# Kernel optimization log

Measured on AMD Instinct MI355X. Metric: run time of the kernel, lower is better.

The kernel has to match this reference:

```python
import jax, jax.numpy as jnp
import numpy as np

N_NODES = 10000
N_EDGES = 160000
HID = 256
NBOND = 6
NATOM = 62
NLAYERS = 6


def _lin_init(key, fan_in, fan_out):
    # torch nn.Linear default: U(-1/sqrt(fan_in), 1/sqrt(fan_in))
    kw, kb = jax.random.split(key)
    bound = 1.0 / np.sqrt(fan_in)
    w = jax.random.uniform(kw, (fan_in, fan_out), jnp.float32, -bound, bound)
    b = jax.random.uniform(kb, (fan_out,), jnp.float32, -bound, bound)
    return w, b


def setup_inputs() -> dict:
    key = jax.random.key(0)
    ks = jax.random.split(key, 32)
    atom_features = jax.random.normal(ks[0], (N_NODES, NATOM), jnp.float32)
    edge_index = jax.random.randint(ks[1], (2, N_EDGES), 0, N_NODES, jnp.int64 if jax.config.jax_enable_x64 else jnp.int32)
    edge_features = jax.random.normal(ks[2], (N_EDGES, NBOND), jnp.float32)

    embed_w, embed_b = _lin_init(ks[3], NATOM, HID)

    msg_in = 2 * HID + NBOND  # 518
    mw1, mb1, mw2, mb2 = [], [], [], []
    uw1, ub1, uw2, ub2 = [], [], [], []
    for i in range(NLAYERS):
        k = jax.random.split(ks[4 + i], 4)
        w, b = _lin_init(k[0], msg_in, HID); mw1.append(w); mb1.append(b)
        w, b = _lin_init(k[1], HID, HID); mw2.append(w); mb2.append(b)
        w, b = _lin_init(k[2], 2 * HID, HID); uw1.append(w); ub1.append(b)
        w, b = _lin_init(k[3], HID, HID); uw2.append(w); ub2.append(b)

    r_w1, r_b1 = _lin_init(ks[20], HID, HID)
    r_w2, r_b2 = _lin_init(ks[21], HID, HID // 2)
    r_w3, r_b3 = _lin_init(ks[22], HID // 2, 1)

    return {
        "atom_features": atom_features,
        "edge_index": edge_index,
        "edge_features": edge_features,
        "embed_w": embed_w, "embed_b": embed_b,
        "msg_w1": jnp.stack(mw1), "msg_b1": jnp.stack(mb1),
        "msg_w2": jnp.stack(mw2), "msg_b2": jnp.stack(mb2),
        "upd_w1": jnp.stack(uw1), "upd_b1": jnp.stack(ub1),
        "upd_w2": jnp.stack(uw2), "upd_b2": jnp.stack(ub2),
        "r_w1": r_w1, "r_b1": r_b1,
        "r_w2": r_w2, "r_b2": r_b2,
        "r_w3": r_w3, "r_b3": r_b3,
    }


def _mlp2(x, w1, b1, w2, b2):
    return jnp.maximum(x @ w1 + b1, 0.0) @ w2 + b2


def reference(atom_features, edge_index, edge_features,
              embed_w, embed_b,
              msg_w1, msg_b1, msg_w2, msg_b2,
              upd_w1, upd_b1, upd_w2, upd_b2,
              r_w1, r_b1, r_w2, r_b2, r_w3, r_b3):
    src, dst = edge_index[0], edge_index[1]
    n = atom_features.shape[0]
    x = atom_features @ embed_w + embed_b  # [N, H]
    for l in range(msg_w1.shape[0]):
        # per-edge gather + concat -> message MLP
        msg_in = jnp.concatenate([x[src], x[dst], edge_features], axis=-1)  # [E, 2H+B]
        msgs = _mlp2(msg_in, msg_w1[l], msg_b1[l], msg_w2[l], msg_b2[l])  # [E, H]
        # scatter-add into dst nodes
        agg = jax.ops.segment_sum(msgs, dst, num_segments=n)  # [N, H]
        x = _mlp2(jnp.concatenate([x, agg], axis=-1), upd_w1[l], upd_b1[l], upd_w2[l], upd_b2[l])
    # readout (dropout is identity in eval mode)
    h = jnp.maximum(x @ r_w1 + r_b1, 0.0)
    h = jnp.maximum(h @ r_w2 + r_b2, 0.0)
    out = h @ r_w3 + r_b3  # [N, 1]
    return out.mean(axis=0)  # [1]
```

## Files before the change

### kernel.cpp

```cpp
#include <hip/hip_runtime.h>
#include <hip/hip_bf16.h>
#include <hip/hip_fp16.h>


#define HID 256

typedef _Float16 h8 __attribute__((ext_vector_type(8)));
typedef float f32x4 __attribute__((ext_vector_type(4)));

__device__ __forceinline__ void unpack_h8(const int4& r, float* f) {
    const __half2* h = reinterpret_cast<const __half2*>(&r);
#pragma unroll
    for (int k = 0; k < 4; ++k) {
        float2 t = __half22float2(h[k]);
        f[2 * k] = t.x;
        f[2 * k + 1] = t.y;
    }
}

__device__ __forceinline__ void gld16(const void* g, void* l) {
    __builtin_amdgcn_global_load_lds(
        (const __attribute__((address_space(1))) void*)g,
        (__attribute__((address_space(3))) void*)l, 16, 0, 0);
}

__device__ __forceinline__ int swz(int row) { return (row + (row >> 2)) & 3; }


__global__ void hist_act_kernel(const int* __restrict__ dst, int* __restrict__ deg,
                                int E, const float* __restrict__ atom,
                                __half* __restrict__ atomH, int NA) {
    int i = blockIdx.x * blockDim.x + threadIdx.x;
    if (i < E) atomicAdd(&deg[dst[i]], 1);
    if (i < NA) {
        int r = i >> 3, seg = i & 7;
        h8 v;
#pragma unroll
        for (int j = 0; j < 8; ++j) {
            int c = seg * 8 + j;
            v[j] = (_Float16)((c < 62) ? atom[(size_t)r * 62 + c] : 0.f);
        }
        *reinterpret_cast<h8*>(&atomH[(size_t)r * 64 + seg * 8]) = v;
    }
}

__global__ __launch_bounds__(256) void scan_kernel(
    const int* __restrict__ deg, int* __restrict__ offs, float* __restrict__ degf, int n) {
    __shared__ int ws[4];
    const int t = threadIdx.x;
    const int lane = t & 63;
    const int w = t >> 6;
    const int per = (n + 255) / 256;
    const int s = t * per;
    const int e = min(s + per, n);
    int sum = 0;
    for (int i = s; i < e; ++i) sum += deg[i];
    int v = sum;
#pragma unroll
    for (int off = 1; off < 64; off <<= 1) {
        int u = __shfl_up(v, off, 64);
        if (lane >= off) v += u;
    }
    if (lane == 63) ws[w] = v;
    __syncthreads();
    if (t == 0) {
        int c = 0;
#pragma unroll
        for (int i = 0; i < 4; ++i) { int x = ws[i]; ws[i] = c; c += x; }
    }
    __syncthreads();
    int run = ws[w] + v - sum;
    for (int i = s; i < e; ++i) {
        int d = deg[i];
        offs[i] = run;
        degf[i] = (float)d;
        run += d;
    }
    if (e == n) offs[n] = run;
}


struct CDesc {
    const float* src;
    __half* dst;
    int Kreal, Kpad, srcN, tile0;
};
struct CTab {
    CDesc d[32];
    int nd;
};

__device__ void convert_body(const CTab& tab, int bid) {
    int idx = 0;
    for (int i = 1; i < tab.nd; ++i)
        if (tab.d[i].tile0 <= bid) idx = i;
    const CDesc d = tab.d[idx];
    const int q = bid - d.tile0;
    const int ntN = d.srcN >> 6;
    const int kb = (q / ntN) * 32;
    const int nb = (q % ntN) * 64;
    const int n = nb + (threadIdx.x & 63);
    const int k0 = kb + (threadIdx.x >> 6) * 8;
    h8 v;
#pragma unroll
    for (int j = 0; j < 8; ++j) {
        int k = k0 + j;
        v[j] = (_Float16)((k < d.Kreal) ? d.src[(size_t)k * d.srcN + n] : 0.f);
    }
    *reinterpret_cast<h8*>(&d.dst[(size_t)n * d.Kpad + k0]) = v;
}

__global__ __launch_bounds__(256) void scatter_conv_kernel(
    const int* __restrict__ src, const int* __restrict__ dst,
    const int* __restrict__ offs, int* __restrict__ cursor,
    int* __restrict__ csr_src, const float* __restrict__ ef,
    __half* __restrict__ ef8, int E, int sblocks, CTab tab) {
    if ((int)blockIdx.x < sblocks) {
        int i = blockIdx.x * blockDim.x + threadIdx.x;
        if (i < E) {
            int d = dst[i];
            int pos = atomicAdd(&cursor[d], 1);
            int idx = offs[d] + pos;
            csr_src[idx] = src[i];
            const float* s6 = ef + (size_t)i * 6;
            unsigned short h[8];
#pragma unroll
            for (int j = 0; j < 6; ++j) h[j] = __half_as_ushort(__float2half_rn(s6[j]));
            h[6] = 0; h[7] = 0;
            int4 pk;
            pk.x = (int)(h[0] | ((unsigned)h[1] << 16));
            pk.y = (int)(h[2] | ((unsigned)h[3] << 16));
            pk.z = (int)(h[4] | ((unsigned)h[5] << 16));
            pk.w = (int)(h[6] | ((unsigned)h[7] << 16));
            *reinterpret_cast<int4*>(ef8 + (size_t)idx * 8) = pk;
        }
    } else {
        convert_body(tab, blockIdx.x - sblocks);
    }
}


struct BDesc { float* out; const float* base; const float* v1; const float* B1;
               const float* v2; const float* B2; };
struct BTab { BDesc d[31]; };


#define ASTR 40

struct FDesc { const float* U2; const __half* Wfb; __half* dst; };
struct FTab { FDesc d[22]; };

__global__ __launch_bounds__(256) void fold_bias_kernel(FTab tab, BTab bt, int fblocks) {
    if ((int)blockIdx.x >= fblocks) {
        const BDesc d = bt.d[blockIdx.x - fblocks];
        const int j = threadIdx.x;
        float acc = d.base ? d.base[j] : 0.f;
        if (d.v1)
            for (int k = 0; k < 256; ++k) acc = fmaf(d.v1[k], d.B1[(size_t)k * 256 + j], acc);
        if (d.v2)
            for (int k = 0; k < 256; ++k) acc = fmaf(d.v2[k], d.B2[(size_t)k * 256 + j], acc);
        d.out[j] = acc;
        return;
    }
    const FDesc dd = tab.d[blockIdx.x >> 4];
    const int t4 = blockIdx.x & 15;
    const int rowBase = (t4 >> 2) * 64;
    const int colBase = (t4 & 3) * 64;

    __shared__ __align__(16) _Float16 Ah[64 * ASTR];
    __shared__ __align__(16) _Float16 Bh[64 * ASTR];

    const int tid = threadIdx.x;
    const int lane = tid & 63;
    const int wave = tid >> 6;
    const int waveM = (wave >> 1) * 32;
    const int waveN = (wave & 1) * 32;
    const int m0 = lane & 15;
    const int quad = lane >> 4;
    const int sr = tid >> 2;
    const int sseg = tid & 3;

    const f32x4 z = {0.f, 0.f, 0.f, 0.f};
    f32x4 acc[2][2] = {{z, z}, {z, z}};

    for (int kb = 0; kb < 256; kb += 32) {
        {
            size_t off = (size_t)(rowBase + sr) * 256 + kb + sseg * 8;
            *reinterpret_cast<int4*>(&Ah[sr * ASTR + sseg * 8]) =
                *reinterpret_cast<const int4*>(&dd.Wfb[off]);
        }
        {
            const float* Bp = dd.U2 + (size_t)(colBase + sr) * 256 + kb + sseg * 8;
            float4 u0 = *reinterpret_cast<const float4*>(Bp);
            float4 u1 = *reinterpret_cast<const float4*>(Bp + 4);
            h8 v;
            v[0] = (_Float16)u0.x; v[1] = (_Float16)u0.y;
            v[2] = (_Float16)u0.z; v[3] = (_Float16)u0.w;
            v[4] = (_Float16)u1.x; v[5] = (_Float16)u1.y;
            v[6] = (_Float16)u1.z; v[7] = (_Float16)u1.w;
            *reinterpret_cast<h8*>(&Bh[sr * ASTR + sseg * 8]) = v;
        }
        __syncthreads();

        const h8 a0 = *reinterpret_cast<const h8*>(&Ah[(waveM + m0) * ASTR + quad * 8]);
        const h8 a1 = *reinterpret_cast<const h8*>(&Ah[(waveM + 16 + m0) * ASTR + quad * 8]);
        const h8 b0 = *reinterpret_cast<const h8*>(&Bh[(waveN + m0) * ASTR + quad * 8]);
        const h8 b1 = *reinterpret_cast<const h8*>(&Bh[(waveN + 16 + m0) * ASTR + quad * 8]);

        acc[0][0] = __builtin_amdgcn_mfma_f32_16x16x32_f16(a0, b0, acc[0][0], 0, 0, 0);
        acc[0][1] = __builtin_amdgcn_mfma_f32_16x16x32_f16(a0, b1, acc[0][1], 0, 0, 0);
        acc[1][0] = __builtin_amdgcn_mfma_f32_16x16x32_f16(a1, b0, acc[1][0], 0, 0, 0);
        acc[1][1] = __builtin_amdgcn_mfma_f32_16x16x32_f16(a1, b1, acc[1][1], 0, 0, 0);

        __syncthreads();
    }

#pragma unroll
    for (int tm = 0; tm < 2; ++tm)
#pragma unroll
        for (int reg = 0; reg < 4; ++reg) {
            int n = rowBase + waveM + tm * 16 + quad * 4 + reg;
#pragma unroll
            for (int tn = 0; tn < 2; ++tn) {
                int k = colBase + waveN + tn * 16 + m0;
                dd.dst[(size_t)n * 256 + k] = __float2half_rn(acc[tm][tn][reg]);
            }
        }
}


template <int TN>
__global__ __launch_bounds__(256) void mfma_gemm(
    const __half* __restrict__ A, int lda,
    const __half* __restrict__ W, int K,
    const float* __restrict__ bias, const float* __restrict__ bias2,
    const float* __restrict__ rowscale,
    const __half* __restrict__ addend, int astride,
    __half* __restrict__ C, int M, int Nc, int do_relu) {
    constexpr int BUF = 4096 + TN * 2048;
    __shared__ __align__(16) unsigned char lds[2 * BUF];

    const int tid = threadIdx.x;
    const int lane = tid & 63;
    const int wave = tid >> 6;
    const int m0 = lane & 15;
    const int quad = lane >> 4;
    const int waveM = (wave >> 1) * 32;
    const int waveN = (wave & 1) * (TN * 16);
    const int rowBase = blockIdx.x * 64;
    const int colBase = blockIdx.y * (TN * 32);

    const int sa_r = tid >> 2;
    const int sa_ks = (tid & 3) ^ swz(sa_r);
    const int sa_row = min(rowBase + sa_r, M - 1);
    const int sb_r1 = sa_r + 64;
    const int sb_ks1 = (tid & 3) ^ swz(sb_r1);

    int aoff[2], boff[TN];
#pragma unroll
    for (int tm = 0; tm < 2; ++tm) {
        int r = waveM + tm * 16 + m0;
        aoff[tm] = ((r << 2) + (quad ^ swz(r))) << 4;
    }
#pragma unroll
    for (int tn = 0; tn < TN; ++tn) {
        int r = waveN + tn * 16 + m0;
        boff[tn] = 4096 + (((r << 2) + (quad ^ swz(r))) << 4);
    }

    const f32x4 z = {0.f, 0.f, 0.f, 0.f};
    f32x4 acc[2][TN];
#pragma unroll
    for (int tm = 0; tm < 2; ++tm)
#pragma unroll
        for (int tn = 0; tn < TN; ++tn) acc[tm][tn] = z;

    const __half* ga = A + (size_t)sa_row * lda + sa_ks * 8;
    const __half* gb0 = W + (size_t)(colBase + sa_r) * K + sa_ks * 8;
    const __half* gb1 = W + (size_t)(colBase + sb_r1) * K + sb_ks1 * 8;

    auto issue = [&](int p, int kb) {
        unsigned char* base = lds + p * BUF;
        gld16(ga + kb, base + wave * 1024);
        gld16(gb0 + kb, base + 4096 + wave * 1024);
        if constexpr (TN == 4) gld16(gb1 + kb, base + 8192 + wave * 1024);
    };

    issue(0, 0);
    int p = 0;
    for (int kb = 0; kb < K; kb += 32) {
        const bool has_next = (kb + 32 < K);
        if (has_next) issue(p ^ 1, kb + 32);
        if (has_next) {
            if constexpr (TN == 4)
                asm volatile("s_waitcnt vmcnt(3)" ::: "memory");
            else
                asm volatile("s_waitcnt vmcnt(2)" ::: "memory");
        } else {
            asm volatile("s_waitcnt vmcnt(0)" ::: "memory");
        }
        asm volatile("s_barrier" ::: "memory");

        const unsigned char* base = lds + p * BUF;
        h8 ah[2], bh[TN];
#pragma unroll
        for (int tm = 0; tm < 2; ++tm)
            ah[tm] = *reinterpret_cast<const h8*>(base + aoff[tm]);
#pragma unroll
        for (int tn = 0; tn < TN; ++tn)
            bh[tn] = *reinterpret_cast<const h8*>(base + boff[tn]);
#pragma unroll
        for (int tm = 0; tm < 2; ++tm)
#pragma unroll
            for (int tn = 0; tn < TN; ++tn)
                acc[tm][tn] = __builtin_amdgcn_mfma_f32_16x16x32_f16(
                    ah[tm], bh[tn], acc[tm][tn], 0, 0, 0);
        asm volatile("s_waitcnt lgkmcnt(0)" ::: "memory");
        asm volatile("s_barrier" ::: "memory");
        p ^= 1;
    }

    float cb[TN], db[TN];
    int col[TN];
#pragma unroll
    for (int tn = 0; tn < TN; ++tn) {
        col[tn] = colBase + waveN + tn * 16 + m0;
        cb[tn] = bias ? bias[col[tn]] : 0.f;
        db[tn] = bias2 ? bias2[col[tn]] : 0.f;
    }
#pragma unroll
    for (int tm = 0; tm < 2; ++tm) {
#pragma unroll
        for (int reg = 0; reg < 4; ++reg) {
            int row = rowBase + waveM + tm * 16 + quad * 4 + reg;
            if (row >= M) continue;
            float rs = rowscale ? rowscale[row] : 0.0f;
#pragma unroll
            for (int tn = 0; tn < TN; ++tn) {
                float v = acc[tm][tn][reg] + cb[tn] + rs * db[tn];
                if (addend)
                    v += __half2float(addend[(size_t)row * astride + col[tn]]);
                if (do_relu) v = fmaxf(v, 0.f);
                C[(size_t)row * Nc + col[tn]] = __float2half_rn(v);
            }
        }
    }
}


__global__ __launch_bounds__(256) void aggregate_kernel(
    const __half* __restrict__ PQ, const __half* __restrict__ ef8,
    const int* __restrict__ offs, const int* __restrict__ csr_src,
    const float* __restrict__ W1c, __half* __restrict__ Hagg, int n) {
    const int wave = threadIdx.x >> 6;
    const int lane = threadIdx.x & 63;
    const int node = blockIdx.x * 4 + wave;
    if (node >= n) return;
    const int hw = lane >> 5;
    const int sl = lane & 31;
    const int ch = sl * 8;

    float wc[6][8];
#pragma unroll
    for (int k = 0; k < 6; ++k) {
        float4 w0 = *reinterpret_cast<const float4*>(W1c + k * HID + ch);
        float4 w1 = *reinterpret_cast<const float4*>(W1c + k * HID + ch + 4);
        wc[k][0] = w0.x; wc[k][1] = w0.y; wc[k][2] = w0.z; wc[k][3] = w0.w;
        wc[k][4] = w1.x; wc[k][5] = w1.y; wc[k][6] = w1.z; wc[k][7] = w1.w;
    }
    float qb[8];
    {
        int4 r = *reinterpret_cast<const int4*>(PQ + (size_t)node * 768 + 256 + ch);
        unpack_h8(r, qb);
    }
    float acc[8] = {0.f, 0.f, 0.f, 0.f, 0.f, 0.f, 0.f, 0.f};

    auto fma_edge = [&](const int4& praw, const int4& eraw) {
        float p[8], e[8];
        unpack_h8(praw, p);
        unpack_h8(eraw, e);
#pragma unroll
        for (int i = 0; i < 8; ++i) {
            float h = p[i] + qb[i];
            h = fmaf(e[0], wc[0][i], h);
            h = fmaf(e[1], wc[1][i], h);
            h = fmaf(e[2], wc[2][i], h);
            h = fmaf(e[3], wc[3][i], h);
            h = fmaf(e[4], wc[4][i], h);
            h = fmaf(e[5], wc[5][i], h);
            acc[i] += fmaxf(h, 0.f);
        }
    };

    const int beg = offs[node];
    const int end = offs[node + 1];
    int j = beg + hw;

    while (j + 10 < end) {
        int s0 = csr_src[j];
        int s1 = csr_src[j + 2];
        int s2 = csr_src[j + 4];
        int s3 = csr_src[j + 6];
        int s4 = csr_src[j + 8];
        int s5 = csr_src[j + 10];
        int4 e0 = *reinterpret_cast<const int4*>(ef8 + (size_t)j * 8);
        int4 e1 = *reinterpret_cast<const int4*>(ef8 + (size_t)(j + 2) * 8);
        int4 e2 = *reinterpret_cast<const int4*>(ef8 + (size_t)(j + 4) * 8);
        int4 e3 = *reinterpret_cast<const int4*>(ef8 + (size_t)(j + 6) * 8);
        int4 e4 = *reinterpret_cast<const int4*>(ef8 + (size_t)(j + 8) * 8);
        int4 e5 = *reinterpret_cast<const int4*>(ef8 + (size_t)(j + 10) * 8);
        int4 p0 = *reinterpret_cast<const int4*>(PQ + (size_t)s0 * 768 + ch);
        int4 p1 = *reinterpret_cast<const int4*>(PQ + (size_t)s1 * 768 + ch);
        int4 p2 = *reinterpret_cast<const int4*>(PQ + (size_t)s2 * 768 + ch);
        int4 p3 = *reinterpret_cast<const int4*>(PQ + (size_t)s3 * 768 + ch);
        int4 p4 = *reinterpret_cast<const int4*>(PQ + (size_t)s4 * 768 + ch);
        int4 p5 = *reinterpret_cast<const int4*>(PQ + (size_t)s5 * 768 + ch);
        fma_edge(p0, e0);
        fma_edge(p1, e1);
        fma_edge(p2, e2);
        fma_edge(p3, e3);
        fma_edge(p4, e4);
        fma_edge(p5, e5);
        j += 12;
    }
    for (; j + 2 < end; j += 4) {
        int s0 = csr_src[j];
        int s1 = csr_src[j + 2];
        int4 e0 = *reinterpret_cast<const int4*>(ef8 + (size_t)j * 8);
        int4 e1 = *reinterpret_cast<const int4*>(ef8 + (size_t)(j + 2) * 8);
        int4 p0 = *reinterpret_cast<const int4*>(PQ + (size_t)s0 * 768 + ch);
        int4 p1 = *reinterpret_cast<const int4*>(PQ + (size_t)s1 * 768 + ch);
        fma_edge(p0, e0);
        fma_edge(p1, e1);
    }
    if (j < end) {
        int s = csr_src[j];
        int4 e = *reinterpret_cast<const int4*>(ef8 + (size_t)j * 8);
        int4 pw = *reinterpret_cast<const int4*>(PQ + (size_t)s * 768 + ch);
        fma_edge(pw, e);
    }

    unsigned short hs[8];
#pragma unroll
    for (int i = 0; i < 8; ++i) {
        float tot = acc[i] + __shfl_down(acc[i], 32, 64);
        hs[i] = __half_as_ushort(__float2half_rn(tot));
    }
    if (hw == 0) {
        int4 pk;
        pk.x = (int)(hs[0] | ((unsigned)hs[1] << 16));
        pk.y = (int)(hs[2] | ((unsigned)hs[3] << 16));
        pk.z = (int)(hs[4] | ((unsigned)hs[5] << 16));
        pk.w = (int)(hs[6] | ((unsigned)hs[7] << 16));
        *reinterpret_cast<int4*>(Hagg + (size_t)node * HID + ch) = pk;
    }
}


__global__ __launch_bounds__(256) void readout_kernel(
    const __half* __restrict__ U5, const __half* __restrict__ wF,
    const float* __restrict__ cbF, const __half* __restrict__ wR2,
    const float* __restrict__ bR2, const float* __restrict__ w3,
    const float* __restrict__ b3, float* __restrict__ accum,
    int* __restrict__ done, float* __restrict__ outp, int M, int nblocks) {
    __shared__ __align__(16) unsigned char lds[24576 + 64 * 272 * 2];
    _Float16* h1 = (_Float16*)(lds + 24576);

    const int tid = threadIdx.x;
    const int lane = tid & 63;
    const int wave = tid >> 6;
    const int m0 = lane & 15;
    const int quad = lane >> 4;
    const int waveM = (wave >> 1) * 32;
    const int waveN = (wave & 1) * 64;
    const int rowBase = blockIdx.x * 64;

    const int sa_r = tid >> 2;
    const int sa_ks = (tid & 3) ^ swz(sa_r);
    const int sa_row = min(rowBase + sa_r, M - 1);
    const int sb_r1 = sa_r + 64;
    const int sb_ks1 = (tid & 3) ^ swz(sb_r1);

    int aoff[2], boff[4];
#pragma unroll
    for (int tm = 0; tm < 2; ++tm) {
        int r = waveM + tm * 16 + m0;
        aoff[tm] = ((r << 2) + (quad ^ swz(r))) << 4;
    }
#pragma unroll
    for (int tn = 0; tn < 4; ++tn) {
        int r = waveN + tn * 16 + m0;
        boff[tn] = (((r << 2) + (quad ^ swz(r))) << 4);
    }

    constexpr int BUF = 4096 + 4 * 2048;
    const f32x4 z = {0.f, 0.f, 0.f, 0.f};

    for (int half = 0; half < 2; ++half) {
        const __half* W = wF + (size_t)(half * 128) * 256;
        f32x4 acc[2][4] = {{z, z, z, z}, {z, z, z, z}};
        const __half* ga = U5 + (size_t)sa_row * 256 + sa_ks * 8;
        const __half* gb0 = W + (size_t)sa_r * 256 + sa_ks * 8;
        const __half* gb1 = W + (size_t)sb_r1 * 256 + sb_ks1 * 8;

        auto issue = [&](int p, int kb) {
            unsigned char* base = lds + p * BUF;
            gld16(ga + kb, base + wave * 1024);
            gld16(gb0 + kb, base + 4096 + wave * 1024);
            gld16(gb1 + kb, base + 8192 + wave * 1024);
        };
        issue(0, 0);
        int p = 0;
        for (int kb = 0; kb < 256; kb += 32) {
            const bool has_next = (kb + 32 < 256);
            if (has_next) issue(p ^ 1, kb + 32);
            if (has_next) asm volatile("s_waitcnt vmcnt(3)" ::: "memory");
            else asm volatile("s_waitcnt vmcnt(0)" ::: "memory");
            asm volatile("s_barrier" ::: "memory");
            const unsigned char* base = lds + p * BUF;
            h8 ah[2], bh[4];
#pragma unroll
            for (int tm = 0; tm < 2; ++tm)
                ah[tm] = *reinterpret_cast<const h8*>(base + aoff[tm]);
#pragma unroll
            for (int tn = 0; tn < 4; ++tn)
                bh[tn] = *reinterpret_cast<const h8*>(base + 4096 + boff[tn]);
#pragma unroll
            for (int tm = 0; tm < 2; ++tm)
#pragma unroll
                for (int tn = 0; tn < 4; ++tn)
                    acc[tm][tn] = __builtin_amdgcn_mfma_f32_16x16x32_f16(
                        ah[tm], bh[tn], acc[tm][tn], 0, 0, 0);
            asm volatile("s_waitcnt lgkmcnt(0)" ::: "memory");
            asm volatile("s_barrier" ::: "memory");
            p ^= 1;
        }
#pragma unroll
        for (int tm = 0; tm < 2; ++tm)
#pragma unroll
            for (int reg = 0; reg < 4; ++reg) {
                int r = waveM + tm * 16 + quad * 4 + reg;
#pragma unroll
                for (int tn = 0; tn < 4; ++tn) {
                    int c = half * 128 + waveN + tn * 16 + m0;
                    float v = acc[tm][tn][reg] + cbF[c];
                    h1[r * 272 + c] = (_Float16)fmaxf(v, 0.f);
                }
            }
        __syncthreads();
    }

    f32x4 acc2[2][4] = {{z, z, z, z}, {z, z, z, z}};
    auto issueB = [&](int p, int kb) {
        unsigned char* base = lds + p * 8192;
        gld16(wR2 + (size_t)sa_r * 256 + sa_ks * 8 + kb, base + wave * 1024);
        gld16(wR2 + (size_t)sb_r1 * 256 + sb_ks1 * 8 + kb, base + 4096 + wave * 1024);
    };
    issueB(0, 0);
    int p = 0;
    for (int kb = 0; kb < 256; kb += 32) {
        const bool has_next = (kb + 32 < 256);
        if (has_next) issueB(p ^ 1, kb + 32);
        if (has_next) asm volatile("s_waitcnt vmcnt(2)" ::: "memory");
        else asm volatile("s_waitcnt vmcnt(0)" ::: "memory");
        asm volatile("s_barrier" ::: "memory");
        const unsigned char* base = lds + p * 8192;
        h8 ah[2], bh[4];
#pragma unroll
        for (int tm = 0; tm < 2; ++tm)
            ah[tm] = *reinterpret_cast<const h8*>(
                &h1[(waveM + tm * 16 + m0) * 272 + kb + quad * 8]);
#pragma unroll
        for (int tn = 0; tn < 4; ++tn)
            bh[tn] = *reinterpret_cast<const h8*>(base + boff[tn]);
#pragma unroll
        for (int tm = 0; tm < 2; ++tm)
#pragma unroll
            for (int tn = 0; tn < 4; ++tn)
                acc2[tm][tn] = __builtin_amdgcn_mfma_f32_16x16x32_f16(
                    ah[tm], bh[tn], acc2[tm][tn], 0, 0, 0);
        asm volatile("s_waitcnt lgkmcnt(0)" ::: "memory");
        asm volatile("s_barrier" ::: "memory");
        p ^= 1;
    }

    float s = 0.f;
#pragma unroll
    for (int tm = 0; tm < 2; ++tm)
#pragma unroll
        for (int reg = 0; reg < 4; ++reg) {
            int row = rowBase + waveM + tm * 16 + quad * 4 + reg;
            if (row >= M) continue;
#pragma unroll
            for (int tn = 0; tn < 4; ++tn) {
                int c = waveN + tn * 16 + m0;
                float v = acc2[tm][tn][reg] + bR2[c];
                s += fmaxf(v, 0.f) * w3[c];
            }
        }
    __syncthreads();
    float* red = (float*)lds;
    red[tid] = s;
    __syncthreads();
    for (int off = 128; off > 0; off >>= 1) {
        if (tid < off) red[tid] += red[tid + off];
        __syncthreads();
    }
    if (tid == 0) {
        atomicAdd(accum, red[0]);
        __threadfence();
        int old = atomicAdd(done, 1);
        if (old == nblocks - 1) {
            float tot = atomicAdd(accum, 0.0f);
            outp[0] = tot / (float)M + b3[0];
        }
    }
}


extern "C" void kernel_launch(void* const* d_in, const int* in_sizes, int n_in,
                              void* d_out, int out_size, void* d_ws, size_t ws_size,
                              hipStream_t stream) {
    const float* atom   = (const float*)d_in[0];
    const int*   eidx   = (const int*)d_in[1];
    const float* ef     = (const float*)d_in[2];
    const float* emb_w  = (const float*)d_in[3];
    const float* emb_b  = (const float*)d_in[4];
    const float* msg_w1 = (const float*)d_in[5];
    const float* msg_b1 = (const float*)d_in[6];
    const float* msg_w2 = (const float*)d_in[7];
    const float* msg_b2 = (const float*)d_in[8];
    const float* upd_w1 = (const float*)d_in[9];
    const float* upd_b1 = (const float*)d_in[10];
    const float* upd_w2 = (const float*)d_in[11];
    const float* upd_b2 = (const float*)d_in[12];
    const float* r_w1   = (const float*)d_in[13];
    const float* r_b1   = (const float*)d_in[14];
    const float* r_w2   = (const float*)d_in[15];
    const float* r_b2   = (const float*)d_in[16];
    const float* r_w3   = (const float*)d_in[17];
    const float* r_b3   = (const float*)d_in[18];

    const int N = in_sizes[0] / 62;
    const int E = in_sizes[1] / 2;
    const int L = in_sizes[5] / (518 * 256);
    const int* src = eidx;
    const int* dst = eidx + E;

    char* wp = (char*)d_ws;
    auto alloc = [&](size_t bytes) -> void* {
        void* p = (void*)wp;
        wp += (bytes + 255) & ~(size_t)255;
        return p;
    };
    int*   deg     = (int*)alloc((size_t)N * 4);
    int*   cursor  = (int*)alloc((size_t)N * 4);
    float* accum   = (float*)alloc(256);
    int*   done    = (int*)((char*)accum + 16);
    size_t zero_bytes = (size_t)((char*)accum - (char*)d_ws) + 256;
    float* degf    = (float*)alloc((size_t)N * 4);
    int*   offs    = (int*)alloc((size_t)(N + 1) * 4);
    int*   csr_src = (int*)alloc((size_t)E * 4);
    __half* ef8    = (__half*)alloc((size_t)E * 8 * 2);

    const int SQ_P = 256 * 256;
    __half* w_emb = (__half*)alloc((size_t)256 * 64 * 2);
    __half* w_r2  = (__half*)alloc((size_t)128 * 256 * 2);
    __half* wF    = (__half*)alloc((size_t)SQ_P * 2);
    __half *wPQR[6], *wM3_[6];
    for (int l = 0; l < L; ++l) {
        wPQR[l] = (__half*)alloc((size_t)768 * 256 * 2);
        wM3_[l] = (__half*)alloc((size_t)SQ_P * 2);
    }
    __half* fb[22];
    for (int i = 0; i < 22; ++i) fb[i] = (__half*)alloc((size_t)SQ_P * 2);
    float* bvec = (float*)alloc((size_t)19 * 256 * 4);
    float* b768 = (float*)alloc((size_t)L * 768 * 4);

    __half* atomH = (__half*)alloc((size_t)N * 64 * 2);
    __half* bufX0 = (__half*)alloc((size_t)N * HID * 2);
    __half* bufX1 = (__half*)alloc((size_t)N * HID * 2);
    __half* PQR   = (__half*)alloc((size_t)N * 768 * 2);
    __half* HaggH = (__half*)alloc((size_t)N * HID * 2);

    hipMemsetAsync(d_ws, 0, zero_bytes, stream);

    const int hag = max(E, N * 8);
    hist_act_kernel<<<(hag + 255) / 256, 256, 0, stream>>>(dst, deg, E, atom, atomH, N * 8);
    scan_kernel<<<1, 256, 0, stream>>>(deg, offs, degf, N);

    CTab ct1;
    int nd = 0, tiles = 0;
    auto addDesc = [&](CTab& ct, const float* s, __half* dh, int Kreal, int Kpad,
                       int srcN) {
        ct.d[nd] = {s, dh, Kreal, Kpad, srcN, tiles};
        tiles += (Kpad / 32) * (srcN / 64);
        ++nd;
    };
    addDesc(ct1, emb_w, w_emb, 62, 64, 256);
    addDesc(ct1, msg_w1, wPQR[0], 256, 256, 256);
    addDesc(ct1, msg_w1 + 256 * 256, wPQR[0] + SQ_P, 256, 256, 256);
    addDesc(ct1, upd_w1, wPQR[0] + 2 * SQ_P, 256, 256, 256);
    addDesc(ct1, r_w2, w_r2, 256, 256, 128);
    for (int l = 1; l < L; ++l) {
        addDesc(ct1, msg_w1 + (size_t)l * 518 * 256,             fb[l - 1], 256, 256, 256);
        addDesc(ct1, msg_w1 + (size_t)l * 518 * 256 + 256 * 256, fb[4 + l], 256, 256, 256);
        addDesc(ct1, upd_w1 + (size_t)l * 512 * 256,             fb[9 + l], 256, 256, 256);
    }
    for (int l = 0; l < L; ++l)
        addDesc(ct1, upd_w1 + (size_t)l * 512 * 256 + 256 * 256, fb[15 + l], 256, 256, 256);
    addDesc(ct1, r_w1, fb[21], 256, 256, 256);
    ct1.nd = nd;

    const int sblocks = (E + 255) / 256;
    scatter_conv_kernel<<<sblocks + tiles, 256, 0, stream>>>(
        src, dst, offs, cursor, csr_src, ef, ef8, E, sblocks, ct1);

    FTab ft;
    for (int l = 1; l < L; ++l) {
        const float* U2p = upd_w2 + (size_t)(l - 1) * SQ_P;
        ft.d[l - 1] = {U2p, fb[l - 1], wPQR[l]};
        ft.d[4 + l] = {U2p, fb[4 + l], wPQR[l] + SQ_P};
        ft.d[9 + l] = {U2p, fb[9 + l], wPQR[l] + 2 * SQ_P};
    }
    for (int l = 0; l < L; ++l)
        ft.d[15 + l] = {msg_w2 + (size_t)l * SQ_P, fb[15 + l], wM3_[l]};
    ft.d[21] = {upd_w2 + (size_t)5 * SQ_P, fb[21], wF};

    BTab bt;
    int nb = 0;
    for (int l = 0; l < L; ++l) {
        const float* ub2p = (l > 0) ? upd_b2 + (size_t)(l - 1) * 256 : nullptr;
        bt.d[nb++] = {b768 + (size_t)l * 768 + 256, msg_b1 + (size_t)l * 256,
                      ub2p, msg_w1 + (size_t)l * 518 * 256,
                      ub2p, msg_w1 + (size_t)l * 518 * 256 + 256 * 256};
        bt.d[nb++] = {b768 + (size_t)l * 768, nullptr, nullptr, nullptr, nullptr, nullptr};
        bt.d[nb++] = {b768 + (size_t)l * 768 + 512, nullptr, nullptr, nullptr, nullptr, nullptr};
        bt.d[nb++] = {bvec + (size_t)(6 + l) * 256, upd_b1 + (size_t)l * 256,
                      ub2p, upd_w1 + (size_t)l * 512 * 256, nullptr, nullptr};
        bt.d[nb++] = {bvec + (size_t)(12 + l) * 256, nullptr,
                      msg_b2 + (size_t)l * 256, upd_w1 + (size_t)l * 512 * 256 + 256 * 256,
                      nullptr, nullptr};
    }
    bt.d[nb++] = {bvec + (size_t)18 * 256, r_b1, upd_b2 + (size_t)5 * 256, r_w1,
                  nullptr, nullptr};
    fold_bias_kernel<<<22 * 16 + nb, 256, 0, stream>>>(ft, bt, 22 * 16);

    const int mblk = (N + 63) / 64;
    dim3 blk(256);

    mfma_gemm<2><<<dim3(mblk, 4), blk, 0, stream>>>(
        atomH, 64, w_emb, 64,
        emb_b, nullptr, nullptr, nullptr, 0,
        bufX0, N, HID, 0);

    __half* U_prev = bufX0;
    __half* U_next = bufX1;
    for (int l = 0; l < L; ++l) {
        const float* w1c = msg_w1 + (size_t)l * 518 * 256 + 512 * 256;

        mfma_gemm<4><<<dim3(mblk, 6), blk, 0, stream>>>(
            U_prev, HID, wPQR[l], HID,
            b768 + (size_t)l * 768, nullptr, nullptr, nullptr, 0,
            PQR, N, 768, 0);
        aggregate_kernel<<<(N + 3) / 4, blk, 0, stream>>>(
            PQR, ef8, offs, csr_src, w1c, HaggH, N);
        mfma_gemm<2><<<dim3(mblk, 4), blk, 0, stream>>>(
            HaggH, HID, wM3_[l], HID,
            bvec + (size_t)(6 + l) * 256, bvec + (size_t)(12 + l) * 256, degf,
            PQR + 512, 768,
            U_next, N, HID, 1);
        __half* t = U_prev; U_prev = U_next; U_next = t;
    }

    readout_kernel<<<mblk, blk, 0, stream>>>(
        U_prev, wF, bvec + (size_t)18 * 256, w_r2, r_b2, r_w3, r_b3,
        accum, done, (float*)d_out, N, mblk);
}
```

Measured before the change: 493.3 us.

## Fuse embedding GEMM into setup kernels, pack src into edge data, merge final update into readout

Several launches are fused. The embedding-weight conversion moves into the histogram kernel, and the embedding GEMM moves into the scatter/convert kernel as extra blocks. The CSR source index is stored in the spare fourth word of each packed edge-feature record, so the aggregate kernel no longer loads a separate csr_src array. The last layer's update GEMM is folded into the readout kernel, which removes one launch and one round trip of the node features. The cost is more LDS in the scatter kernel and a longer readout kernel with an extra GEMM stage.

```diff
diff --git a/kernel.cpp b/kernel.cpp
--- a/kernel.cpp
+++ b/kernel.cpp
@@ -29,7 +29,22 @@
 
 __global__ void hist_act_kernel(const int* __restrict__ dst, int* __restrict__ deg,
                                 int E, const float* __restrict__ atom,
-                                __half* __restrict__ atomH, int NA) {
+                                __half* __restrict__ atomH, int NA, int hblocks,
+                                const float* __restrict__ emb_w,
+                                __half* __restrict__ w_emb) {
+    if ((int)blockIdx.x >= hblocks) {
+        int q = blockIdx.x - hblocks;
+        int n = (q & 3) * 64 + (threadIdx.x & 63);
+        int k0 = (q >> 2) * 32 + (threadIdx.x >> 6) * 8;
+        h8 v;
+#pragma unroll
+        for (int j = 0; j < 8; ++j) {
+            int k = k0 + j;
+            v[j] = (_Float16)((k < 62) ? emb_w[(size_t)k * 256 + n] : 0.f);
+        }
+        *reinterpret_cast<h8*>(&w_emb[(size_t)n * 64 + k0]) = v;
+        return;
+    }
     int i = blockIdx.x * blockDim.x + threadIdx.x;
     if (i < E) atomicAdd(&deg[dst[i]], 1);
     if (i < NA) {
@@ -110,135 +125,17 @@
     *reinterpret_cast<h8*>(&d.dst[(size_t)n * d.Kpad + k0]) = v;
 }
 
-__global__ __launch_bounds__(256) void scatter_conv_kernel(
-    const int* __restrict__ src, const int* __restrict__ dst,
-    const int* __restrict__ offs, int* __restrict__ cursor,
-    int* __restrict__ csr_src, const float* __restrict__ ef,
-    __half* __restrict__ ef8, int E, int sblocks, CTab tab) {
-    if ((int)blockIdx.x < sblocks) {
-        int i = blockIdx.x * blockDim.x + threadIdx.x;
-        if (i < E) {
-            int d = dst[i];
-            int pos = atomicAdd(&cursor[d], 1);
-            int idx = offs[d] + pos;
-            csr_src[idx] = src[i];
-            const float* s6 = ef + (size_t)i * 6;
-            unsigned short h[8];
-#pragma unroll
-            for (int j = 0; j < 6; ++j) h[j] = __half_as_ushort(__float2half_rn(s6[j]));
-            h[6] = 0; h[7] = 0;
-            int4 pk;
-            pk.x = (int)(h[0] | ((unsigned)h[1] << 16));
-            pk.y = (int)(h[2] | ((unsigned)h[3] << 16));
-            pk.z = (int)(h[4] | ((unsigned)h[5] << 16));
-            pk.w = (int)(h[6] | ((unsigned)h[7] << 16));
-            *reinterpret_cast<int4*>(ef8 + (size_t)idx * 8) = pk;
-        }
-    } else {
-        convert_body(tab, blockIdx.x - sblocks);
-    }
-}
-
-
-struct BDesc { float* out; const float* base; const float* v1; const float* B1;
-               const float* v2; const float* B2; };
-struct BTab { BDesc d[31]; };
-
-
-#define ASTR 40
-
-struct FDesc { const float* U2; const __half* Wfb; __half* dst; };
-struct FTab { FDesc d[22]; };
-
-__global__ __launch_bounds__(256) void fold_bias_kernel(FTab tab, BTab bt, int fblocks) {
-    if ((int)blockIdx.x >= fblocks) {
-        const BDesc d = bt.d[blockIdx.x - fblocks];
-        const int j = threadIdx.x;
-        float acc = d.base ? d.base[j] : 0.f;
-        if (d.v1)
-            for (int k = 0; k < 256; ++k) acc = fmaf(d.v1[k], d.B1[(size_t)k * 256 + j], acc);
-        if (d.v2)
-            for (int k = 0; k < 256; ++k) acc = fmaf(d.v2[k], d.B2[(size_t)k * 256 + j], acc);
-        d.out[j] = acc;
-        return;
-    }
-    const FDesc dd = tab.d[blockIdx.x >> 4];
-    const int t4 = blockIdx.x & 15;
-    const int rowBase = (t4 >> 2) * 64;
-    const int colBase = (t4 & 3) * 64;
-
-    __shared__ __align__(16) _Float16 Ah[64 * ASTR];
-    __shared__ __align__(16) _Float16 Bh[64 * ASTR];
-
-    const int tid = threadIdx.x;
-    const int lane = tid & 63;
-    const int wave = tid >> 6;
-    const int waveM = (wave >> 1) * 32;
-    const int waveN = (wave & 1) * 32;
-    const int m0 = lane & 15;
-    const int quad = lane >> 4;
-    const int sr = tid >> 2;
-    const int sseg = tid & 3;
-
-    const f32x4 z = {0.f, 0.f, 0.f, 0.f};
-    f32x4 acc[2][2] = {{z, z}, {z, z}};
-
-    for (int kb = 0; kb < 256; kb += 32) {
-        {
-            size_t off = (size_t)(rowBase + sr) * 256 + kb + sseg * 8;
-            *reinterpret_cast<int4*>(&Ah[sr * ASTR + sseg * 8]) =
-                *reinterpret_cast<const int4*>(&dd.Wfb[off]);
-        }
-        {
-            const float* Bp = dd.U2 + (size_t)(colBase + sr) * 256 + kb + sseg * 8;
-            float4 u0 = *reinterpret_cast<const float4*>(Bp);
-            float4 u1 = *reinterpret_cast<const float4*>(Bp + 4);
-            h8 v;
-            v[0] = (_Float16)u0.x; v[1] = (_Float16)u0.y;
-            v[2] = (_Float16)u0.z; v[3] = (_Float16)u0.w;
-            v[4] = (_Float16)u1.x; v[5] = (_Float16)u1.y;
-            v[6] = (_Float16)u1.z; v[7] = (_Float16)u1.w;
-            *reinterpret_cast<h8*>(&Bh[sr * ASTR + sseg * 8]) = v;
-        }
-        __syncthreads();
-
-        const h8 a0 = *reinterpret_cast<const h8*>(&Ah[(waveM + m0) * ASTR + quad * 8]);
-        const h8 a1 = *reinterpret_cast<const h8*>(&Ah[(waveM + 16 + m0) * ASTR + quad * 8]);
-        const h8 b0 = *reinterpret_cast<const h8*>(&Bh[(waveN + m0) * ASTR + quad * 8]);
-        const h8 b1 = *reinterpret_cast<const h8*>(&Bh[(waveN + 16 + m0) * ASTR + quad * 8]);
-
-        acc[0][0] = __builtin_amdgcn_mfma_f32_16x16x32_f16(a0, b0, acc[0][0], 0, 0, 0);
-        acc[0][1] = __builtin_amdgcn_mfma_f32_16x16x32_f16(a0, b1, acc[0][1], 0, 0, 0);
-        acc[1][0] = __builtin_amdgcn_mfma_f32_16x16x32_f16(a1, b0, acc[1][0], 0, 0, 0);
-        acc[1][1] = __builtin_amdgcn_mfma_f32_16x16x32_f16(a1, b1, acc[1][1], 0, 0, 0);
-
-        __syncthreads();
-    }
-
-#pragma unroll
-    for (int tm = 0; tm < 2; ++tm)
-#pragma unroll
-        for (int reg = 0; reg < 4; ++reg) {
-            int n = rowBase + waveM + tm * 16 + quad * 4 + reg;
-#pragma unroll
-            for (int tn = 0; tn < 2; ++tn) {
-                int k = colBase + waveN + tn * 16 + m0;
-                dd.dst[(size_t)n * 256 + k] = __float2half_rn(acc[tm][tn][reg]);
-            }
-        }
-}
-
 
 template <int TN>
-__global__ __launch_bounds__(256) void mfma_gemm(
+__device__ void gemm_body(unsigned char* lds,
     const __half* __restrict__ A, int lda,
     const __half* __restrict__ W, int K,
     const float* __restrict__ bias, const float* __restrict__ bias2,
     const float* __restrict__ rowscale,
     const __half* __restrict__ addend, int astride,
-    __half* __restrict__ C, int M, int Nc, int do_relu) {
+    __half* __restrict__ C, int M, int Nc, int do_relu,
+    int rowBase, int colBase) {
     constexpr int BUF = 4096 + TN * 2048;
-    __shared__ __align__(16) unsigned char lds[2 * BUF];
 
     const int tid = threadIdx.x;
     const int lane = tid & 63;
@@ -247,8 +144,6 @@
     const int quad = lane >> 4;
     const int waveM = (wave >> 1) * 32;
     const int waveN = (wave & 1) * (TN * 16);
-    const int rowBase = blockIdx.x * 64;
-    const int colBase = blockIdx.y * (TN * 32);
 
     const int sa_r = tid >> 2;
     const int sa_ks = (tid & 3) ^ swz(sa_r);
@@ -347,11 +242,153 @@
     }
 }
 
+template <int TN>
+__global__ __launch_bounds__(256) void mfma_gemm(
+    const __half* __restrict__ A, int lda,
+    const __half* __restrict__ W, int K,
+    const float* __restrict__ bias, const float* __restrict__ bias2,
+    const float* __restrict__ rowscale,
+    const __half* __restrict__ addend, int astride,
+    __half* __restrict__ C, int M, int Nc, int do_relu) {
+    constexpr int BUF = 4096 + TN * 2048;
+    __shared__ __align__(16) unsigned char lds[2 * BUF];
+    gemm_body<TN>(lds, A, lda, W, K, bias, bias2, rowscale, addend, astride,
+                  C, M, Nc, do_relu, blockIdx.x * 64, blockIdx.y * (TN * 32));
+}
+
+
+__global__ __launch_bounds__(256) void scatter_conv_kernel(
+    const int* __restrict__ src, const int* __restrict__ dst,
+    const int* __restrict__ offs, int* __restrict__ cursor,
+    const float* __restrict__ ef, __half* __restrict__ ef8,
+    int E, int sblocks, int tiles, CTab tab,
+    const __half* __restrict__ atomH, const __half* __restrict__ w_emb,
+    const float* __restrict__ emb_b, __half* __restrict__ X0, int M, int mblk) {
+    __shared__ __align__(16) unsigned char lds[2 * (4096 + 2 * 2048)];
+    const int bid = blockIdx.x;
+    if (bid < sblocks) {
+        int i = bid * blockDim.x + threadIdx.x;
+        if (i < E) {
+            int d = dst[i];
+            int pos = atomicAdd(&cursor[d], 1);
+            int idx = offs[d] + pos;
+            const float* s6 = ef + (size_t)i * 6;
+            unsigned short h[6];
+#pragma unroll
+            for (int j = 0; j < 6; ++j) h[j] = __half_as_ushort(__float2half_rn(s6[j]));
+            int4 pk;
+            pk.x = (int)(h[0] | ((unsigned)h[1] << 16));
+            pk.y = (int)(h[2] | ((unsigned)h[3] << 16));
+            pk.z = (int)(h[4] | ((unsigned)h[5] << 16));
+            pk.w = src[i];
+            *reinterpret_cast<int4*>(ef8 + (size_t)idx * 8) = pk;
+        }
+    } else if (bid < sblocks + tiles) {
+        convert_body(tab, bid - sblocks);
+    } else {
+        int q = bid - sblocks - tiles;
+        int bx = q % mblk;
+        int by = q / mblk;
+        gemm_body<2>(lds, atomH, 64, w_emb, 64,
+                     emb_b, nullptr, nullptr, nullptr, 0,
+                     X0, M, 256, 0, bx * 64, by * 64);
+    }
+}
+
+
+struct BDesc { float* out; const float* base; const float* v1; const float* B1;
+               const float* v2; const float* B2; };
+struct BTab { BDesc d[31]; };
+
+
+#define ASTR 40
+
+struct FDesc { const float* U2; const __half* Wfb; __half* dst; };
+struct FTab { FDesc d[22]; };
+
+__global__ __launch_bounds__(256) void fold_bias_kernel(FTab tab, BTab bt, int fblocks) {
+    if ((int)blockIdx.x >= fblocks) {
+        const BDesc d = bt.d[blockIdx.x - fblocks];
+        const int j = threadIdx.x;
+        float acc = d.base ? d.base[j] : 0.f;
+        if (d.v1)
+            for (int k = 0; k < 256; ++k) acc = fmaf(d.v1[k], d.B1[(size_t)k * 256 + j], acc);
+        if (d.v2)
+            for (int k = 0; k < 256; ++k) acc = fmaf(d.v2[k], d.B2[(size_t)k * 256 + j], acc);
+        d.out[j] = acc;
+        return;
+    }
+    const FDesc dd = tab.d[blockIdx.x >> 4];
+    const int t4 = blockIdx.x & 15;
+    const int rowBase = (t4 >> 2) * 64;
+    const int colBase = (t4 & 3) * 64;
+
+    __shared__ __align__(16) _Float16 Ah[64 * ASTR];
+    __shared__ __align__(16) _Float16 Bh[64 * ASTR];
+
+    const int tid = threadIdx.x;
+    const int lane = tid & 63;
+    const int wave = tid >> 6;
+    const int waveM = (wave >> 1) * 32;
+    const int waveN = (wave & 1) * 32;
+    const int m0 = lane & 15;
+    const int quad = lane >> 4;
+    const int sr = tid >> 2;
+    const int sseg = tid & 3;
+
+    const f32x4 z = {0.f, 0.f, 0.f, 0.f};
+    f32x4 acc[2][2] = {{z, z}, {z, z}};
+
+    for (int kb = 0; kb < 256; kb += 32) {
+        {
+            size_t off = (size_t)(rowBase + sr) * 256 + kb + sseg * 8;
+            *reinterpret_cast<int4*>(&Ah[sr * ASTR + sseg * 8]) =
+                *reinterpret_cast<const int4*>(&dd.Wfb[off]);
+        }
+        {
+            const float* Bp = dd.U2 + (size_t)(colBase + sr) * 256 + kb + sseg * 8;
+            float4 u0 = *reinterpret_cast<const float4*>(Bp);
+            float4 u1 = *reinterpret_cast<const float4*>(Bp + 4);
+            h8 v;
+            v[0] = (_Float16)u0.x; v[1] = (_Float16)u0.y;
+            v[2] = (_Float16)u0.z; v[3] = (_Float16)u0.w;
+            v[4] = (_Float16)u1.x; v[5] = (_Float16)u1.y;
+            v[6] = (_Float16)u1.z; v[7] = (_Float16)u1.w;
+            *reinterpret_cast<h8*>(&Bh[sr * ASTR + sseg * 8]) = v;
+        }
+        __syncthreads();
+
+        const h8 a0 = *reinterpret_cast<const h8*>(&Ah[(waveM + m0) * ASTR + quad * 8]);
+        const h8 a1 = *reinterpret_cast<const h8*>(&Ah[(waveM + 16 + m0) * ASTR + quad * 8]);
+        const h8 b0 = *reinterpret_cast<const h8*>(&Bh[(waveN + m0) * ASTR + quad * 8]);
+        const h8 b1 = *reinterpret_cast<const h8*>(&Bh[(waveN + 16 + m0) * ASTR + quad * 8]);
+
+        acc[0][0] = __builtin_amdgcn_mfma_f32_16x16x32_f16(a0, b0, acc[0][0], 0, 0, 0);
+        acc[0][1] = __builtin_amdgcn_mfma_f32_16x16x32_f16(a0, b1, acc[0][1], 0, 0, 0);
+        acc[1][0] = __builtin_amdgcn_mfma_f32_16x16x32_f16(a1, b0, acc[1][0], 0, 0, 0);
+        acc[1][1] = __builtin_amdgcn_mfma_f32_16x16x32_f16(a1, b1, acc[1][1], 0, 0, 0);
+
+        __syncthreads();
+    }
+
+#pragma unroll
+    for (int tm = 0; tm < 2; ++tm)
+#pragma unroll
+        for (int reg = 0; reg < 4; ++reg) {
+            int n = rowBase + waveM + tm * 16 + quad * 4 + reg;
+#pragma unroll
+            for (int tn = 0; tn < 2; ++tn) {
+                int k = colBase + waveN + tn * 16 + m0;
+                dd.dst[(size_t)n * 256 + k] = __float2half_rn(acc[tm][tn][reg]);
+            }
+        }
+}
+
 
 __global__ __launch_bounds__(256) void aggregate_kernel(
     const __half* __restrict__ PQ, const __half* __restrict__ ef8,
-    const int* __restrict__ offs, const int* __restrict__ csr_src,
-    const float* __restrict__ W1c, __half* __restrict__ Hagg, int n) {
+    const int* __restrict__ offs, const float* __restrict__ W1c,
+    __half* __restrict__ Hagg, int n) {
     const int wave = threadIdx.x >> 6;
     const int lane = threadIdx.x & 63;
     const int node = blockIdx.x * 4 + wave;
@@ -376,9 +413,16 @@
     float acc[8] = {0.f, 0.f, 0.f, 0.f, 0.f, 0.f, 0.f, 0.f};
 
     auto fma_edge = [&](const int4& praw, const int4& eraw) {
-        float p[8], e[8];
+        float p[8], e[6];
         unpack_h8(praw, p);
-        unpack_h8(eraw, e);
+        {
+            const __half2* hh = reinterpret_cast<const __half2*>(&eraw);
+            float2 t0 = __half22float2(hh[0]);
+            float2 t1 = __half22float2(hh[1]);
+            float2 t2 = __half22float2(hh[2]);
+            e[0] = t0.x; e[1] = t0.y; e[2] = t1.x; e[3] = t1.y;
+            e[4] = t2.x; e[5] = t2.y;
+        }
 #pragma unroll
         for (int i = 0; i < 8; ++i) {
             float h = p[i] + qb[i];
@@ -397,24 +441,18 @@
     int j = beg + hw;
 
     while (j + 10 < end) {
-        int s0 = csr_src[j];
-        int s1 = csr_src[j + 2];
-        int s2 = csr_src[j + 4];
-        int s3 = csr_src[j + 6];
-        int s4 = csr_src[j + 8];
-        int s5 = csr_src[j + 10];
         int4 e0 = *reinterpret_cast<const int4*>(ef8 + (size_t)j * 8);
         int4 e1 = *reinterpret_cast<const int4*>(ef8 + (size_t)(j + 2) * 8);
         int4 e2 = *reinterpret_cast<const int4*>(ef8 + (size_t)(j + 4) * 8);
         int4 e3 = *reinterpret_cast<const int4*>(ef8 + (size_t)(j + 6) * 8);
         int4 e4 = *reinterpret_cast<const int4*>(ef8 + (size_t)(j + 8) * 8);
         int4 e5 = *reinterpret_cast<const int4*>(ef8 + (size_t)(j + 10) * 8);
-        int4 p0 = *reinterpret_cast<const int4*>(PQ + (size_t)s0 * 768 + ch);
-        int4 p1 = *reinterpret_cast<const int4*>(PQ + (size_t)s1 * 768 + ch);
-        int4 p2 = *reinterpret_cast<const int4*>(PQ + (size_t)s2 * 768 + ch);
-        int4 p3 = *reinterpret_cast<const int4*>(PQ + (size_t)s3 * 768 + ch);
-        int4 p4 = *reinterpret_cast<const int4*>(PQ + (size_t)s4 * 768 + ch);
-        int4 p5 = *reinterpret_cast<const int4*>(PQ + (size_t)s5 * 768 + ch);
+        int4 p0 = *reinterpret_cast<const int4*>(PQ + (size_t)e0.w * 768 + ch);
+        int4 p1 = *reinterpret_cast<const int4*>(PQ + (size_t)e1.w * 768 + ch);
+        int4 p2 = *reinterpret_cast<const int4*>(PQ + (size_t)e2.w * 768 + ch);
+        int4 p3 = *reinterpret_cast<const int4*>(PQ + (size_t)e3.w * 768 + ch);
+        int4 p4 = *reinterpret_cast<const int4*>(PQ + (size_t)e4.w * 768 + ch);
+        int4 p5 = *reinterpret_cast<const int4*>(PQ + (size_t)e5.w * 768 + ch);
         fma_edge(p0, e0);
         fma_edge(p1, e1);
         fma_edge(p2, e2);
@@ -424,19 +462,16 @@
         j += 12;
     }
     for (; j + 2 < end; j += 4) {
-        int s0 = csr_src[j];
-        int s1 = csr_src[j + 2];
         int4 e0 = *reinterpret_cast<const int4*>(ef8 + (size_t)j * 8);
         int4 e1 = *reinterpret_cast<const int4*>(ef8 + (size_t)(j + 2) * 8);
-        int4 p0 = *reinterpret_cast<const int4*>(PQ + (size_t)s0 * 768 + ch);
-        int4 p1 = *reinterpret_cast<const int4*>(PQ + (size_t)s1 * 768 + ch);
+        int4 p0 = *reinterpret_cast<const int4*>(PQ + (size_t)e0.w * 768 + ch);
+        int4 p1 = *reinterpret_cast<const int4*>(PQ + (size_t)e1.w * 768 + ch);
         fma_edge(p0, e0);
         fma_edge(p1, e1);
     }
     if (j < end) {
-        int s = csr_src[j];
         int4 e = *reinterpret_cast<const int4*>(ef8 + (size_t)j * 8);
-        int4 pw = *reinterpret_cast<const int4*>(PQ + (size_t)s * 768 + ch);
+        int4 pw = *reinterpret_cast<const int4*>(PQ + (size_t)e.w * 768 + ch);
         fma_edge(pw, e);
     }
 
@@ -458,13 +493,16 @@
 
 
 __global__ __launch_bounds__(256) void readout_kernel(
-    const __half* __restrict__ U5, const __half* __restrict__ wF,
-    const float* __restrict__ cbF, const __half* __restrict__ wR2,
-    const float* __restrict__ bR2, const float* __restrict__ w3,
-    const float* __restrict__ b3, float* __restrict__ accum,
-    int* __restrict__ done, float* __restrict__ outp, int M, int nblocks) {
+    const __half* __restrict__ Hagg, const __half* __restrict__ wM3,
+    const float* __restrict__ cbU, const float* __restrict__ dbU,
+    const float* __restrict__ degf, const __half* __restrict__ Radd,
+    const __half* __restrict__ wF, const float* __restrict__ cbF,
+    const __half* __restrict__ wR2, const float* __restrict__ bR2,
+    const float* __restrict__ w3, const float* __restrict__ b3,
+    float* __restrict__ accum, int* __restrict__ done,
+    float* __restrict__ outp, int M, int nblocks) {
     __shared__ __align__(16) unsigned char lds[24576 + 64 * 272 * 2];
-    _Float16* h1 = (_Float16*)(lds + 24576);
+    _Float16* UH = (_Float16*)(lds + 24576);
 
     const int tid = threadIdx.x;
     const int lane = tid & 63;
@@ -497,9 +535,9 @@
     const f32x4 z = {0.f, 0.f, 0.f, 0.f};
 
     for (int half = 0; half < 2; ++half) {
-        const __half* W = wF + (size_t)(half * 128) * 256;
+        const __half* W = wM3 + (size_t)(half * 128) * 256;
         f32x4 acc[2][4] = {{z, z, z, z}, {z, z, z, z}};
-        const __half* ga = U5 + (size_t)sa_row * 256 + sa_ks * 8;
+        const __half* ga = Hagg + (size_t)sa_row * 256 + sa_ks * 8;
         const __half* gb0 = W + (size_t)sa_r * 256 + sa_ks * 8;
         const __half* gb1 = W + (size_t)sb_r1 * 256 + sb_ks1 * 8;
 
@@ -539,28 +577,90 @@
         for (int tm = 0; tm < 2; ++tm)
 #pragma unroll
             for (int reg = 0; reg < 4; ++reg) {
-                int r = waveM + tm * 16 + quad * 4 + reg;
+                int rl = waveM + tm * 16 + quad * 4 + reg;
+                int rr = min(rowBase + rl, M - 1);
+                float rs = degf[rr];
 #pragma unroll
                 for (int tn = 0; tn < 4; ++tn) {
                     int c = half * 128 + waveN + tn * 16 + m0;
-                    float v = acc[tm][tn][reg] + cbF[c];
-                    h1[r * 272 + c] = (_Float16)fmaxf(v, 0.f);
+                    float v = acc[tm][tn][reg] + cbU[c] + rs * dbU[c] +
+                              __half2float(Radd[(size_t)rr * 768 + c]);
+                    UH[rl * 272 + c] = (_Float16)fmaxf(v, 0.f);
                 }
             }
         __syncthreads();
     }
 
+    f32x4 accH[2][2][4];
+#pragma unroll
+    for (int hf = 0; hf < 2; ++hf)
+#pragma unroll
+        for (int tm = 0; tm < 2; ++tm)
+#pragma unroll
+            for (int tn = 0; tn < 4; ++tn) accH[hf][tm][tn] = z;
+    for (int half = 0; half < 2; ++half) {
+        const __half* W = wF + (size_t)(half * 128) * 256;
+        auto issueB = [&](int p, int kb) {
+            unsigned char* base = lds + p * 8192;
+            gld16(W + (size_t)sa_r * 256 + sa_ks * 8 + kb, base + wave * 1024);
+            gld16(W + (size_t)sb_r1 * 256 + sb_ks1 * 8 + kb, base + 4096 + wave * 1024);
+        };
+        issueB(0, 0);
+        int p = 0;
+        for (int kb = 0; kb < 256; kb += 32) {
+            const bool has_next = (kb + 32 < 256);
+            if (has_next) issueB(p ^ 1, kb + 32);
+            if (has_next) asm volatile("s_waitcnt vmcnt(2)" ::: "memory");
+            else asm volatile("s_waitcnt vmcnt(0)" ::: "memory");
+            asm volatile("s_barrier" ::: "memory");
+            const unsigned char* base = lds + p * 8192;
+            h8 ah[2], bh[4];
+#pragma unroll
+            for (int tm = 0; tm < 2; ++tm)
+                ah[tm] = *reinterpret_cast<const h8*>(
+                    &UH[(waveM + tm * 16 + m0) * 272 + kb + quad * 8]);
+#pragma unroll
+            for (int tn = 0; tn < 4; ++tn)
+                bh[tn] = *reinterpret_cast<const h8*>(base + boff[tn]);
+#pragma unroll
+            for (int tm = 0; tm < 2; ++tm)
+#pragma unroll
+                for (int tn = 0; tn < 4; ++tn)
+                    accH[half][tm][tn] = __builtin_amdgcn_mfma_f32_16x16x32_f16(
+                        ah[tm], bh[tn], accH[half][tm][tn], 0, 0, 0);
+            asm volatile("s_waitcnt lgkmcnt(0)" ::: "memory");
+            asm volatile("s_barrier" ::: "memory");
+            p ^= 1;
+        }
+    }
+    __syncthreads();
+#pragma unroll
+    for (int half = 0; half < 2; ++half)
+#pragma unroll
+        for (int tm = 0; tm < 2; ++tm)
+#pragma unroll
+            for (int reg = 0; reg < 4; ++reg) {
+                int rl = waveM + tm * 16 + quad * 4 + reg;
+#pragma unroll
+                for (int tn = 0; tn < 4; ++tn) {
+                    int c = half * 128 + waveN + tn * 16 + m0;
+                    float v = accH[half][tm][tn][reg] + cbF[c];
+                    UH[rl * 272 + c] = (_Float16)fmaxf(v, 0.f);
+                }
+            }
+    __syncthreads();
+
     f32x4 acc2[2][4] = {{z, z, z, z}, {z, z, z, z}};
-    auto issueB = [&](int p, int kb) {
+    auto issueB2 = [&](int p, int kb) {
         unsigned char* base = lds + p * 8192;
         gld16(wR2 + (size_t)sa_r * 256 + sa_ks * 8 + kb, base + wave * 1024);
         gld16(wR2 + (size_t)sb_r1 * 256 + sb_ks1 * 8 + kb, base + 4096 + wave * 1024);
     };
-    issueB(0, 0);
+    issueB2(0, 0);
     int p = 0;
     for (int kb = 0; kb < 256; kb += 32) {
         const bool has_next = (kb + 32 < 256);
-        if (has_next) issueB(p ^ 1, kb + 32);
+        if (has_next) issueB2(p ^ 1, kb + 32);
         if (has_next) asm volatile("s_waitcnt vmcnt(2)" ::: "memory");
         else asm volatile("s_waitcnt vmcnt(0)" ::: "memory");
         asm volatile("s_barrier" ::: "memory");
@@ -569,7 +669,7 @@
 #pragma unroll
         for (int tm = 0; tm < 2; ++tm)
             ah[tm] = *reinterpret_cast<const h8*>(
-                &h1[(waveM + tm * 16 + m0) * 272 + kb + quad * 8]);
+                &UH[(waveM + tm * 16 + m0) * 272 + kb + quad * 8]);
 #pragma unroll
         for (int tn = 0; tn < 4; ++tn)
             bh[tn] = *reinterpret_cast<const h8*>(base + boff[tn]);
@@ -644,8 +744,8 @@
     const int N = in_sizes[0] / 62;
     const int E = in_sizes[1] / 2;
     const int L = in_sizes[5] / (518 * 256);
-    const int* src = eidx;
-    const int* dst = eidx + E;
+    const int* srcp = eidx;
+    const int* dstp = eidx + E;
 
     char* wp = (char*)d_ws;
     auto alloc = [&](size_t bytes) -> void* {
@@ -660,7 +760,6 @@
     size_t zero_bytes = (size_t)((char*)accum - (char*)d_ws) + 256;
     float* degf    = (float*)alloc((size_t)N * 4);
     int*   offs    = (int*)alloc((size_t)(N + 1) * 4);
-    int*   csr_src = (int*)alloc((size_t)E * 4);
     __half* ef8    = (__half*)alloc((size_t)E * 8 * 2);
 
     const int SQ_P = 256 * 256;
@@ -686,7 +785,9 @@
     hipMemsetAsync(d_ws, 0, zero_bytes, stream);
 
     const int hag = max(E, N * 8);
-    hist_act_kernel<<<(hag + 255) / 256, 256, 0, stream>>>(dst, deg, E, atom, atomH, N * 8);
+    const int hblocks = (hag + 255) / 256;
+    hist_act_kernel<<<hblocks + 8, 256, 0, stream>>>(dstp, deg, E, atom, atomH,
+                                                     N * 8, hblocks, emb_w, w_emb);
     scan_kernel<<<1, 256, 0, stream>>>(deg, offs, degf, N);
 
     CTab ct1;
@@ -697,7 +798,6 @@
         tiles += (Kpad / 32) * (srcN / 64);
         ++nd;
     };
-    addDesc(ct1, emb_w, w_emb, 62, 64, 256);
     addDesc(ct1, msg_w1, wPQR[0], 256, 256, 256);
     addDesc(ct1, msg_w1 + 256 * 256, wPQR[0] + SQ_P, 256, 256, 256);
     addDesc(ct1, upd_w1, wPQR[0] + 2 * SQ_P, 256, 256, 256);
@@ -712,9 +812,11 @@
     addDesc(ct1, r_w1, fb[21], 256, 256, 256);
     ct1.nd = nd;
 
+    const int mblk = (N + 63) / 64;
     const int sblocks = (E + 255) / 256;
-    scatter_conv_kernel<<<sblocks + tiles, 256, 0, stream>>>(
-        src, dst, offs, cursor, csr_src, ef, ef8, E, sblocks, ct1);
+    scatter_conv_kernel<<<sblocks + tiles + mblk * 4, 256, 0, stream>>>(
+        srcp, dstp, offs, cursor, ef, ef8, E, sblocks, tiles, ct1,
+        atomH, w_emb, emb_b, bufX0, N, mblk);
 
     FTab ft;
     for (int l = 1; l < L; ++l) {
@@ -746,13 +848,7 @@
                   nullptr, nullptr};
     fold_bias_kernel<<<22 * 16 + nb, 256, 0, stream>>>(ft, bt, 22 * 16);
 
-    const int mblk = (N + 63) / 64;
     dim3 blk(256);
-
-    mfma_gemm<2><<<dim3(mblk, 4), blk, 0, stream>>>(
-        atomH, 64, w_emb, 64,
-        emb_b, nullptr, nullptr, nullptr, 0,
-        bufX0, N, HID, 0);
 
     __half* U_prev = bufX0;
     __half* U_next = bufX1;
@@ -764,16 +860,21 @@
             b768 + (size_t)l * 768, nullptr, nullptr, nullptr, 0,
             PQR, N, 768, 0);
         aggregate_kernel<<<(N + 3) / 4, blk, 0, stream>>>(
-            PQR, ef8, offs, csr_src, w1c, HaggH, N);
-        mfma_gemm<2><<<dim3(mblk, 4), blk, 0, stream>>>(
-            HaggH, HID, wM3_[l], HID,
-            bvec + (size_t)(6 + l) * 256, bvec + (size_t)(12 + l) * 256, degf,
-            PQR + 512, 768,
-            U_next, N, HID, 1);
-        __half* t = U_prev; U_prev = U_next; U_next = t;
+            PQR, ef8, offs, w1c, HaggH, N);
+        if (l < L - 1) {
+            mfma_gemm<2><<<dim3(mblk, 4), blk, 0, stream>>>(
+                HaggH, HID, wM3_[l], HID,
+                bvec + (size_t)(6 + l) * 256, bvec + (size_t)(12 + l) * 256, degf,
+                PQR + 512, 768,
+                U_next, N, HID, 1);
+            __half* t = U_prev; U_prev = U_next; U_next = t;
+        }
     }
 
     readout_kernel<<<mblk, blk, 0, stream>>>(
-        U_prev, wF, bvec + (size_t)18 * 256, w_r2, r_b2, r_w3, r_b3,
+        HaggH, wM3_[L - 1],
+        bvec + (size_t)(6 + (L - 1)) * 256, bvec + (size_t)(12 + (L - 1)) * 256,
+        degf, PQR + 512,
+        wF, bvec + (size_t)18 * 256, w_r2, r_b2, r_w3, r_b3,
         accum, done, (float*)d_out, N, mblk);
 }
```

Result: no change. 499.0 us (+1.2%).
